# Optimization experiments

Measured on AMD Instinct MI355X. Metric: run time of the kernel, lower is better.

Reference implementation:

```python
import jax, jax.numpy as jnp
import numpy as np

FEAT, NHID, NHALF, NCLS = 256, 512, 256, 2

def _xavier(key, shape):
    fan_in, fan_out = shape[0], shape[1]
    limit = np.sqrt(6.0 / (fan_in + fan_out))
    return jax.random.uniform(key, shape, jnp.float32, -limit, limit)

def setup_inputs() -> dict:
    key = jax.random.key(0)
    ks = jax.random.split(key, 10)
    B, N = 64, 1024
    x = jax.random.normal(ks[0], (B, N, FEAT), jnp.float32)
    adj = jax.random.uniform(ks[1], (B, N, N), jnp.float32)
    adj = adj / jnp.sum(adj, axis=-1, keepdims=True)  # row-normalized (mean aggregation)
    return {
        "x": x, "adj": adj,
        "W1": _xavier(ks[2], (2 * FEAT, NHID)), "b1": jnp.zeros((NHID,), jnp.float32),
        "W2": _xavier(ks[3], (2 * NHID, NHID)), "b2": jnp.zeros((NHID,), jnp.float32),
        "W3": _xavier(ks[4], (2 * NHID, NHALF)), "b3": jnp.zeros((NHALF,), jnp.float32),
        "W4": _xavier(ks[5], (2 * NHALF, NHALF)), "b4": jnp.zeros((NHALF,), jnp.float32),
        "Wc1": _xavier(ks[6], (NHALF, NHALF)), "bc1": jnp.zeros((NHALF,), jnp.float32),
        "alpha": jnp.full((NHALF,), 0.25, jnp.float32),  # PReLU per-channel slope
        "Wc2": _xavier(ks[7], (NHALF, NCLS)), "bc2": jnp.zeros((NCLS,), jnp.float32),
    }

def _gconv(x, adj, W, b):
    # MeanAggregator: bmm(adj, x); GraphConv: relu(cat([x, agg]) @ W + b)
    agg = jnp.einsum('bnm,bmd->bnd', adj, x)
    cat = jnp.concatenate([x, agg], axis=-1)
    return jax.nn.relu(jnp.einsum('bnd,df->bnf', cat, W) + b)

def reference(x, adj, W1, b1, W2, b2, W3, b3, W4, b4, Wc1, bc1, alpha, Wc2, bc2):
    h = _gconv(x, adj, W1, b1)
    h = _gconv(h, adj, W2, b2)
    h = _gconv(h, adj, W3, b3)
    h = _gconv(h, adj, W4, b4)
    h = h.reshape(-1, h.shape[-1])  # [B*N, nhid_half]
    h = h @ Wc1 + bc1
    h = jnp.where(h > 0, h, alpha * h)  # PReLU
    logits = h @ Wc2 + bc2
    return jax.nn.log_softmax(logits, axis=-1)
```

## Files before the change

kernel.cpp:

```cpp
#include <hip/hip_runtime.h>
#include <hip/hip_bf16.h>
#include <cmath>

typedef _Float16 f16;
typedef __attribute__((ext_vector_type(4))) _Float16 f16x4;
typedef __attribute__((ext_vector_type(8))) _Float16 f16x8;
typedef __attribute__((ext_vector_type(4))) float f32x4;

__device__ inline void gload_lds16(const f16* g, f16* l) {
  __builtin_amdgcn_global_load_lds(
      (const __attribute__((address_space(1))) unsigned int*)g,
      (__attribute__((address_space(3))) unsigned int*)l, 16, 0, 0);
}

__global__ __launch_bounds__(256) void cvt_f32_f16(const float* __restrict__ in,
                                                   f16* __restrict__ out, long n) {
  long stride = (long)gridDim.x * 256 * 8;
  for (long i = ((long)blockIdx.x * 256 + threadIdx.x) * 8; i < n; i += stride) {
    float4 a = *(const float4*)(in + i);
    float4 b = *(const float4*)(in + i + 4);
    f16x8 o;
    o[0] = (f16)a.x; o[1] = (f16)a.y; o[2] = (f16)a.z; o[3] = (f16)a.w;
    o[4] = (f16)b.x; o[5] = (f16)b.y; o[6] = (f16)b.z; o[7] = (f16)b.w;
    *(f16x8*)(out + i) = o;
  }
}

__global__ __launch_bounds__(256) void transpose_cvt(const float* __restrict__ in,
                                                     f16* __restrict__ out,
                                                     int R, int C, long sIn, long sOut) {
  in  += (long)blockIdx.z * sIn;
  out += (long)blockIdx.z * sOut;
  __shared__ f16 t[32][34];
  const int tx = threadIdx.x, ty = threadIdx.y;
  const int c0 = blockIdx.x * 32, r0 = blockIdx.y * 32;
  #pragma unroll
  for (int j = 0; j < 32; j += 8)
    t[ty + j][tx] = (f16)in[(long)(r0 + ty + j) * C + (c0 + tx)];
  __syncthreads();
  #pragma unroll
  for (int j = 0; j < 32; j += 8)
    out[(long)(c0 + ty + j) * R + (r0 + tx)] = t[tx][ty + j];
}

template <int ACT, bool DUAL, bool WRITE_T>
__global__ __launch_bounds__(512, 2) void gemm256(
    const f16* __restrict__ A1, int lda1,
    const f16* __restrict__ B1, int ldb1, int k1,
    const f16* __restrict__ A2, int lda2,
    const f16* __restrict__ B2, int ldb2, int k2,
    const float* __restrict__ bias, const float* __restrict__ alpha,
    f16* __restrict__ C, int ldc, f16* __restrict__ CT,
    long sA, long sB, long sC) {
  __shared__ f16 As[2][16384];
  __shared__ f16 Bs[2][16384];
  const int tid = threadIdx.x;
  const int z = blockIdx.z;
  const f16* a1 = A1 + (long)z * sA;
  const f16* b1 = B1 + (long)z * sB;
  f16* pC = C + (long)z * sC;
  const int m0 = blockIdx.x * 256, n0 = blockIdx.y * 256;
  const int lane = tid & 63, w = tid >> 6;
  const int wr = w >> 2, wc = w & 3;
  const int lrow = lane & 15, kg = lane >> 4;
  const int NT1 = k1 >> 6;
  const int NT = NT1 + (DUAL ? (k2 >> 6) : 0);

  const int srow = tid >> 3;
  const int cg = (tid & 7) ^ (srow & 7);
  const int ldst = (tid & 448) * 8;

  const int swz = lrow & 7;
  const int ac0 = ((0 * 4 + kg) ^ swz) * 8;
  const int ac1 = ((4 + kg) ^ swz) * 8;
  const int arow = wr * 128 + lrow;
  const int brow = wc * 64 + lrow;

  f32x4 acc[8][4] = {};

  auto stage = [&](int kt) {
    const f16 *Ab, *Bb; int la, lb, kk;
    if (!DUAL || kt < NT1) { Ab = a1; Bb = b1; la = lda1; lb = ldb1; kk = kt << 6; }
    else { Ab = A2; Bb = B2; la = lda2; lb = ldb2; kk = (kt - NT1) << 6; }
    const int bs = kt & 1;
    #pragma unroll
    for (int j = 0; j < 4; ++j)
      gload_lds16(Ab + (long)(m0 + srow + j * 64) * la + kk + cg * 8,
                  &As[bs][j * 4096 + ldst]);
    #pragma unroll
    for (int j = 0; j < 4; ++j)
      gload_lds16(Bb + (long)(n0 + srow + j * 64) * lb + kk + cg * 8,
                  &Bs[bs][j * 4096 + ldst]);
  };

  stage(0);
  stage(1);
  asm volatile("s_waitcnt vmcnt(8)\n\ts_barrier" ::: "memory");

  for (int t = 0; t < NT; ++t) {
    const int bs = t & 1;
    f16x8 af[8], bf[4];
    #pragma unroll
    for (int m = 0; m < 8; ++m)
      af[m] = *(const f16x8*)&As[bs][(arow + m * 16) * 64 + ac0];
    #pragma unroll
    for (int n = 0; n < 4; ++n)
      bf[n] = *(const f16x8*)&Bs[bs][(brow + n * 16) * 64 + ac0];
    __builtin_amdgcn_s_setprio(1);
    #pragma unroll
    for (int m = 0; m < 8; ++m)
      #pragma unroll
      for (int n = 0; n < 4; ++n)
        acc[m][n] = __builtin_amdgcn_mfma_f32_16x16x32_f16(af[m], bf[n], acc[m][n], 0, 0, 0);
    __builtin_amdgcn_s_setprio(0);
    f16x8 ag[8], bg[4];
    #pragma unroll
    for (int m = 0; m < 8; ++m)
      ag[m] = *(const f16x8*)&As[bs][(arow + m * 16) * 64 + ac1];
    #pragma unroll
    for (int n = 0; n < 4; ++n)
      bg[n] = *(const f16x8*)&Bs[bs][(brow + n * 16) * 64 + ac1];
    asm volatile("s_waitcnt lgkmcnt(0)\n\ts_barrier" ::: "memory");
    if (t + 2 < NT) stage(t + 2);
    __builtin_amdgcn_s_setprio(1);
    #pragma unroll
    for (int m = 0; m < 8; ++m)
      #pragma unroll
      for (int n = 0; n < 4; ++n)
        acc[m][n] = __builtin_amdgcn_mfma_f32_16x16x32_f16(ag[m], bg[n], acc[m][n], 0, 0, 0);
    __builtin_amdgcn_s_setprio(0);
    if (t + 2 < NT)
      asm volatile("s_waitcnt vmcnt(8)\n\ts_barrier" ::: "memory");
    else if (t + 1 < NT)
      asm volatile("s_waitcnt vmcnt(0)\n\ts_barrier" ::: "memory");
  }

  #pragma unroll
  for (int n = 0; n < 4; ++n) {
    const int gn = n0 + wc * 64 + n * 16 + lrow;
    const float bv = bias ? bias[gn] : 0.0f;
    const float av = (ACT == 2) ? alpha[gn] : 0.0f;
    #pragma unroll
    for (int m = 0; m < 8; ++m) {
      const int rg0 = m0 + wr * 128 + m * 16 + kg * 4;
      f16 tv[4];
      #pragma unroll
      for (int r = 0; r < 4; ++r) {
        float v = acc[m][n][r] + bv;
        if (ACT == 1) v = fmaxf(v, 0.0f);
        if (ACT == 2) v = (v > 0.0f) ? v : av * v;
        const f16 h = (f16)v;
        tv[r] = h;
        pC[(long)(rg0 + r) * ldc + gn] = h;
      }
      if (WRITE_T) {
        const int b = rg0 >> 10, node = rg0 & 1023;
        f16x4 pk;
        pk[0] = tv[0]; pk[1] = tv[1]; pk[2] = tv[2]; pk[3] = tv[3];
        *(f16x4*)&CT[((long)b * ldc + gn) * 1024 + node] = pk;
      }
    }
  }
}

__global__ __launch_bounds__(256) void logits_lsm(const f16* __restrict__ hc,
                                                  const float* __restrict__ Wc2,
                                                  const float* __restrict__ bc2,
                                                  float* __restrict__ out) {
  __shared__ float w[512];
  __shared__ float bb[2];
  const int t = threadIdx.x;
  w[t] = Wc2[t];
  w[t + 256] = Wc2[t + 256];
  if (t < 2) bb[t] = bc2[t];
  __syncthreads();
  const long row = (long)blockIdx.x * 256 + t;
  const f16* hr = hc + row * 256;
  float l0 = 0.f, l1 = 0.f;
  #pragma unroll 4
  for (int d0 = 0; d0 < 256; d0 += 8) {
    f16x8 v = *(const f16x8*)(hr + d0);
    #pragma unroll
    for (int j = 0; j < 8; ++j) {
      const float p = (float)v[j];
      l0 += p * w[(d0 + j) * 2];
      l1 += p * w[(d0 + j) * 2 + 1];
    }
  }
  l0 += bb[0];
  l1 += bb[1];
  const float mx = fmaxf(l0, l1);
  const float lse = mx + logf(expf(l0 - mx) + expf(l1 - mx));
  out[row * 2] = l0 - lse;
  out[row * 2 + 1] = l1 - lse;
}

extern "C" void kernel_launch(void* const* d_in, const int* in_sizes, int n_in,
                              void* d_out, int out_size, void* d_ws, size_t ws_size,
                              hipStream_t stream) {
  const float* x     = (const float*)d_in[0];
  const float* adj   = (const float*)d_in[1];
  const float* W1    = (const float*)d_in[2];
  const float* b1    = (const float*)d_in[3];
  const float* W2    = (const float*)d_in[4];
  const float* b2    = (const float*)d_in[5];
  const float* W3    = (const float*)d_in[6];
  const float* b3    = (const float*)d_in[7];
  const float* W4    = (const float*)d_in[8];
  const float* b4    = (const float*)d_in[9];
  const float* Wc1   = (const float*)d_in[10];
  const float* bc1   = (const float*)d_in[11];
  const float* alpha = (const float*)d_in[12];
  const float* Wc2   = (const float*)d_in[13];
  const float* bc2   = (const float*)d_in[14];
  float* out = (float*)d_out;

  char* ws = (char*)d_ws;
  f16* adjB = (f16*)(ws + 0L);
  f16* xN   = (f16*)(ws + 134217728L);
  f16* xT   = (f16*)(ws + 167772160L);
  f16* agg  = (f16*)(ws + 201326592L);
  f16* hAN  = (f16*)(ws + 268435456L);
  f16* hAT  = (f16*)(ws + 335544320L);
  f16* hBN  = (f16*)(ws + 402653184L);
  f16* hBT  = (f16*)(ws + 469762048L);
  f16* WT1  = (f16*)(ws + 536870912L);
  f16* WT2  = (f16*)(ws + 537395200L);
  f16* WT3  = (f16*)(ws + 538443776L);
  f16* WT4  = (f16*)(ws + 538968064L);
  f16* WTc1 = (f16*)(ws + 539230208L);
  if (ws_size < (size_t)539361280L) return;

  const dim3 tb(32, 8, 1);

  cvt_f32_f16<<<2048, 256, 0, stream>>>(adj, adjB, 64L * 1024 * 1024);
  cvt_f32_f16<<<1024, 256, 0, stream>>>(x, xN, 64L * 1024 * 256);
  transpose_cvt<<<dim3(8, 32, 64), tb, 0, stream>>>(x, xT, 1024, 256, 1024L * 256, 256L * 1024);
  transpose_cvt<<<dim3(16, 16, 1), tb, 0, stream>>>(W1, WT1, 512, 512, 0, 0);
  transpose_cvt<<<dim3(16, 32, 1), tb, 0, stream>>>(W2, WT2, 1024, 512, 0, 0);
  transpose_cvt<<<dim3(8, 32, 1), tb, 0, stream>>>(W3, WT3, 1024, 256, 0, 0);
  transpose_cvt<<<dim3(8, 16, 1), tb, 0, stream>>>(W4, WT4, 512, 256, 0, 0);
  transpose_cvt<<<dim3(8, 8, 1), tb, 0, stream>>>(Wc1, WTc1, 256, 256, 0, 0);

  gemm256<0, false, false><<<dim3(4, 1, 64), 512, 0, stream>>>(
      adjB, 1024, xT, 1024, 1024,
      nullptr, 0, nullptr, 0, 0,
      nullptr, nullptr, agg, 256, nullptr,
      1024L * 1024, 256L * 1024, 1024L * 256);
  gemm256<1, true, true><<<dim3(256, 2, 1), 512, 0, stream>>>(
      xN, 256, WT1, 512, 256,
      agg, 256, WT1 + 256, 512, 256,
      b1, nullptr, hAN, 512, hAT, 0, 0, 0);

  gemm256<0, false, false><<<dim3(4, 2, 64), 512, 0, stream>>>(
      adjB, 1024, hAT, 1024, 1024,
      nullptr, 0, nullptr, 0, 0,
      nullptr, nullptr, agg, 512, nullptr,
      1024L * 1024, 512L * 1024, 1024L * 512);
  gemm256<1, true, true><<<dim3(256, 2, 1), 512, 0, stream>>>(
      hAN, 512, WT2, 1024, 512,
      agg, 512, WT2 + 512, 1024, 512,
      b2, nullptr, hBN, 512, hBT, 0, 0, 0);

  gemm256<0, false, false><<<dim3(4, 2, 64), 512, 0, stream>>>(
      adjB, 1024, hBT, 1024, 1024,
      nullptr, 0, nullptr, 0, 0,
      nullptr, nullptr, agg, 512, nullptr,
      1024L * 1024, 512L * 1024, 1024L * 512);
  gemm256<1, true, true><<<dim3(256, 1, 1), 512, 0, stream>>>(
      hBN, 512, WT3, 1024, 512,
      agg, 512, WT3 + 512, 1024, 512,
      b3, nullptr, hAN, 256, hAT, 0, 0, 0);

  gemm256<0, false, false><<<dim3(4, 1, 64), 512, 0, stream>>>(
      adjB, 1024, hAT, 1024, 1024,
      nullptr, 0, nullptr, 0, 0,
      nullptr, nullptr, agg, 256, nullptr,
      1024L * 1024, 256L * 1024, 1024L * 256);
  gemm256<1, true, false><<<dim3(256, 1, 1), 512, 0, stream>>>(
      hAN, 256, WT4, 512, 256,
      agg, 256, WT4 + 256, 512, 256,
      b4, nullptr, hBN, 256, nullptr, 0, 0, 0);

  gemm256<2, false, false><<<dim3(256, 1, 1), 512, 0, stream>>>(
      hBN, 256, WTc1, 256, 256,
      nullptr, 0, nullptr, 0, 0,
      bc1, alpha, hAN, 256, nullptr, 0, 0, 0);

  logits_lsm<<<256, 256, 0, stream>>>(hAN, Wc2, bc2, out);
}
```

Measured before the change: 1.125 ms.

## Restructure GEMM main loop into four barrier-synced phases and remap workgroups across XCDs

The GEMM main loop now runs in four smaller phases, each doing a 4x4 MFMA block with its own LDS fragment reads. A and B tile loads are issued at different points in the loop so global-to-LDS traffic overlaps with compute, and the barrier/waitcnt pattern keeps waves in lockstep. The grid is flattened to 1D and block IDs are remapped so consecutive tiles of the same batch and row land on the same XCD, which should improve L2 reuse. The cost is many more barriers per iteration and fewer fragments held in registers at once, so latency hiding may suffer.

New measurement: 1.134 ms. No clear change (+0.8%).

```diff
diff --git a/kernel.cpp b/kernel.cpp
--- a/kernel.cpp
+++ b/kernel.cpp
@@ -43,6 +43,23 @@
     out[(long)(c0 + ty + j) * R + (r0 + tx)] = t[tx][ty + j];
 }
 
+#define MM16(AF, BF, MB)                                                        \
+  do {                                                                          \
+    __builtin_amdgcn_s_setprio(1);                                              \
+    _Pragma("unroll") for (int m_ = 0; m_ < 4; ++m_)                            \
+        _Pragma("unroll") for (int n_ = 0; n_ < 4; ++n_)                        \
+            acc[(MB) + m_][n_] = __builtin_amdgcn_mfma_f32_16x16x32_f16(        \
+                (AF)[m_], (BF)[n_], acc[(MB) + m_][n_], 0, 0, 0);               \
+    __builtin_amdgcn_s_setprio(0);                                              \
+  } while (0)
+
+#define PHASE_SYNC()                                                            \
+  do {                                                                          \
+    __builtin_amdgcn_s_barrier();                                               \
+    asm volatile("s_waitcnt lgkmcnt(0)" ::: "memory");                          \
+    __builtin_amdgcn_sched_barrier(0);                                          \
+  } while (0)
+
 template <int ACT, bool DUAL, bool WRITE_T>
 __global__ __launch_bounds__(512, 2) void gemm256(
     const f16* __restrict__ A1, int lda1,
@@ -51,15 +68,20 @@
     const f16* __restrict__ B2, int ldb2, int k2,
     const float* __restrict__ bias, const float* __restrict__ alpha,
     f16* __restrict__ C, int ldc, f16* __restrict__ CT,
-    long sA, long sB, long sC) {
-  __shared__ f16 As[2][16384];
-  __shared__ f16 Bs[2][16384];
+    long sA, long sB, long sC, int gxs, int gys, int nwg) {
+  __shared__ __align__(16) f16 As[2][16384];
+  __shared__ __align__(16) f16 Bs[2][16384];
+  const int wg = blockIdx.x;
+  const int lid = (wg & 7) * (nwg >> 3) + (wg >> 3);
+  const int bx = lid & ((1 << gxs) - 1);
+  const int by = (lid >> gxs) & ((1 << gys) - 1);
+  const int z = lid >> (gxs + gys);
+
   const int tid = threadIdx.x;
-  const int z = blockIdx.z;
   const f16* a1 = A1 + (long)z * sA;
   const f16* b1 = B1 + (long)z * sB;
   f16* pC = C + (long)z * sC;
-  const int m0 = blockIdx.x * 256, n0 = blockIdx.y * 256;
+  const int m0 = bx * 256, n0 = by * 256;
   const int lane = tid & 63, w = tid >> 6;
   const int wr = w >> 2, wc = w & 3;
   const int lrow = lane & 15, kg = lane >> 4;
@@ -71,68 +93,77 @@
   const int ldst = (tid & 448) * 8;
 
   const int swz = lrow & 7;
-  const int ac0 = ((0 * 4 + kg) ^ swz) * 8;
+  const int ac0 = (kg ^ swz) * 8;
   const int ac1 = ((4 + kg) ^ swz) * 8;
   const int arow = wr * 128 + lrow;
   const int brow = wc * 64 + lrow;
 
   f32x4 acc[8][4] = {};
-
-  auto stage = [&](int kt) {
-    const f16 *Ab, *Bb; int la, lb, kk;
-    if (!DUAL || kt < NT1) { Ab = a1; Bb = b1; la = lda1; lb = ldb1; kk = kt << 6; }
-    else { Ab = A2; Bb = B2; la = lda2; lb = ldb2; kk = (kt - NT1) << 6; }
-    const int bs = kt & 1;
+  int bs = 0;
+
+  auto stageA = [&](int kt) {
+    const f16* Ab; int la, kk;
+    if (!DUAL || kt < NT1) { Ab = a1; la = lda1; kk = kt << 6; }
+    else { Ab = A2; la = lda2; kk = (kt - NT1) << 6; }
+    const int b = kt & 1;
     #pragma unroll
     for (int j = 0; j < 4; ++j)
       gload_lds16(Ab + (long)(m0 + srow + j * 64) * la + kk + cg * 8,
-                  &As[bs][j * 4096 + ldst]);
+                  &As[b][j * 4096 + ldst]);
+  };
+  auto stageB = [&](int kt) {
+    const f16* Bb; int lb, kk;
+    if (!DUAL || kt < NT1) { Bb = b1; lb = ldb1; kk = kt << 6; }
+    else { Bb = B2; lb = ldb2; kk = (kt - NT1) << 6; }
+    const int b = kt & 1;
     #pragma unroll
     for (int j = 0; j < 4; ++j)
       gload_lds16(Bb + (long)(n0 + srow + j * 64) * lb + kk + cg * 8,
-                  &Bs[bs][j * 4096 + ldst]);
+                  &Bs[b][j * 4096 + ldst]);
   };
-
-  stage(0);
-  stage(1);
-  asm volatile("s_waitcnt vmcnt(8)\n\ts_barrier" ::: "memory");
+  auto rdB = [&](f16x8* bf, int ac) {
+    #pragma unroll
+    for (int n = 0; n < 4; ++n)
+      bf[n] = *(const f16x8*)&Bs[bs][(brow + n * 16) * 64 + ac];
+  };
+  auto rdA = [&](f16x8* af, int mo, int ac) {
+    #pragma unroll
+    for (int m = 0; m < 4; ++m)
+      af[m] = *(const f16x8*)&As[bs][(arow + mo + m * 16) * 64 + ac];
+  };
+
+  stageA(0); stageB(0); stageB(1);
+  asm volatile("s_waitcnt vmcnt(4)" ::: "memory");
+  __builtin_amdgcn_s_barrier();
 
   for (int t = 0; t < NT; ++t) {
-    const int bs = t & 1;
-    f16x8 af[8], bf[4];
-    #pragma unroll
-    for (int m = 0; m < 8; ++m)
-      af[m] = *(const f16x8*)&As[bs][(arow + m * 16) * 64 + ac0];
-    #pragma unroll
-    for (int n = 0; n < 4; ++n)
-      bf[n] = *(const f16x8*)&Bs[bs][(brow + n * 16) * 64 + ac0];
-    __builtin_amdgcn_s_setprio(1);
-    #pragma unroll
-    for (int m = 0; m < 8; ++m)
-      #pragma unroll
-      for (int n = 0; n < 4; ++n)
-        acc[m][n] = __builtin_amdgcn_mfma_f32_16x16x32_f16(af[m], bf[n], acc[m][n], 0, 0, 0);
-    __builtin_amdgcn_s_setprio(0);
-    f16x8 ag[8], bg[4];
-    #pragma unroll
-    for (int m = 0; m < 8; ++m)
-      ag[m] = *(const f16x8*)&As[bs][(arow + m * 16) * 64 + ac1];
-    #pragma unroll
-    for (int n = 0; n < 4; ++n)
-      bg[n] = *(const f16x8*)&Bs[bs][(brow + n * 16) * 64 + ac1];
-    asm volatile("s_waitcnt lgkmcnt(0)\n\ts_barrier" ::: "memory");
-    if (t + 2 < NT) stage(t + 2);
-    __builtin_amdgcn_s_setprio(1);
-    #pragma unroll
-    for (int m = 0; m < 8; ++m)
-      #pragma unroll
-      for (int n = 0; n < 4; ++n)
-        acc[m][n] = __builtin_amdgcn_mfma_f32_16x16x32_f16(ag[m], bg[n], acc[m][n], 0, 0, 0);
-    __builtin_amdgcn_s_setprio(0);
-    if (t + 2 < NT)
-      asm volatile("s_waitcnt vmcnt(8)\n\ts_barrier" ::: "memory");
-    else if (t + 1 < NT)
-      asm volatile("s_waitcnt vmcnt(0)\n\ts_barrier" ::: "memory");
+    bs = t & 1;
+    f16x8 bf0[4], bf1[4], af[4];
+    if (t + 1 < NT) stageA(t + 1);
+    rdB(bf0, ac0); rdA(af, 0, ac0);
+    PHASE_SYNC();
+    MM16(af, bf0, 0);
+    __builtin_amdgcn_s_barrier();
+    rdB(bf1, ac1); rdA(af, 0, ac1);
+    PHASE_SYNC();
+    MM16(af, bf1, 0);
+    __builtin_amdgcn_s_barrier();
+    if (t + 2 < NT) stageB(t + 2);
+    rdA(af, 64, ac0);
+    PHASE_SYNC();
+    MM16(af, bf0, 4);
+    __builtin_amdgcn_s_barrier();
+    rdA(af, 64, ac1);
+    PHASE_SYNC();
+    MM16(af, bf1, 4);
+    __builtin_amdgcn_s_barrier();
+    if (t + 1 < NT) {
+      if (t + 2 < NT)
+        asm volatile("s_waitcnt vmcnt(4)" ::: "memory");
+      else
+        asm volatile("s_waitcnt vmcnt(0)" ::: "memory");
+      __builtin_amdgcn_s_barrier();
+    }
   }
 
   #pragma unroll
@@ -242,50 +273,50 @@
   transpose_cvt<<<dim3(8, 16, 1), tb, 0, stream>>>(W4, WT4, 512, 256, 0, 0);
   transpose_cvt<<<dim3(8, 8, 1), tb, 0, stream>>>(Wc1, WTc1, 256, 256, 0, 0);
 
-  gemm256<0, false, false><<<dim3(4, 1, 64), 512, 0, stream>>>(
+  gemm256<0, false, false><<<256, 512, 0, stream>>>(
       adjB, 1024, xT, 1024, 1024,
       nullptr, 0, nullptr, 0, 0,
       nullptr, nullptr, agg, 256, nullptr,
-      1024L * 1024, 256L * 1024, 1024L * 256);
-  gemm256<1, true, true><<<dim3(256, 2, 1), 512, 0, stream>>>(
+      1024L * 1024, 256L * 1024, 1024L * 256, 2, 0, 256);
+  gemm256<1, true, true><<<512, 512, 0, stream>>>(
       xN, 256, WT1, 512, 256,
       agg, 256, WT1 + 256, 512, 256,
-      b1, nullptr, hAN, 512, hAT, 0, 0, 0);
-
-  gemm256<0, false, false><<<dim3(4, 2, 64), 512, 0, stream>>>(
+      b1, nullptr, hAN, 512, hAT, 0, 0, 0, 8, 1, 512);
+
+  gemm256<0, false, false><<<512, 512, 0, stream>>>(
       adjB, 1024, hAT, 1024, 1024,
       nullptr, 0, nullptr, 0, 0,
       nullptr, nullptr, agg, 512, nullptr,
-      1024L * 1024, 512L * 1024, 1024L * 512);
-  gemm256<1, true, true><<<dim3(256, 2, 1), 512, 0, stream>>>(
+      1024L * 1024, 512L * 1024, 1024L * 512, 2, 1, 512);
+  gemm256<1, true, true><<<512, 512, 0, stream>>>(
       hAN, 512, WT2, 1024, 512,
       agg, 512, WT2 + 512, 1024, 512,
-      b2, nullptr, hBN, 512, hBT, 0, 0, 0);
-
-  gemm256<0, false, false><<<dim3(4, 2, 64), 512, 0, stream>>>(
+      b2, nullptr, hBN, 512, hBT, 0, 0, 0, 8, 1, 512);
+
+  gemm256<0, false, false><<<512, 512, 0, stream>>>(
       adjB, 1024, hBT, 1024, 1024,
       nullptr, 0, nullptr, 0, 0,
       nullptr, nullptr, agg, 512, nullptr,
-      1024L * 1024, 512L * 1024, 1024L * 512);
-  gemm256<1, true, true><<<dim3(256, 1, 1), 512, 0, stream>>>(
+      1024L * 1024, 512L * 1024, 1024L * 512, 2, 1, 512);
+  gemm256<1, true, true><<<256, 512, 0, stream>>>(
       hBN, 512, WT3, 1024, 512,
       agg, 512, WT3 + 512, 1024, 512,
-      b3, nullptr, hAN, 256, hAT, 0, 0, 0);
-
-  gemm256<0, false, false><<<dim3(4, 1, 64), 512, 0, stream>>>(
+      b3, nullptr, hAN, 256, hAT, 0, 0, 0, 8, 0, 256);
+
+  gemm256<0, false, false><<<256, 512, 0, stream>>>(
       adjB, 1024, hAT, 1024, 1024,
       nullptr, 0, nullptr, 0, 0,
       nullptr, nullptr, agg, 256, nullptr,
-      1024L * 1024, 256L * 1024, 1024L * 256);
-  gemm256<1, true, false><<<dim3(256, 1, 1), 512, 0, stream>>>(
+      1024L * 1024, 256L * 1024, 1024L * 256, 2, 0, 256);
+  gemm256<1, true, false><<<256, 512, 0, stream>>>(
       hAN, 256, WT4, 512, 256,
       agg, 256, WT4 + 256, 512, 256,
-      b4, nullptr, hBN, 256, nullptr, 0, 0, 0);
-
-  gemm256<2, false, false><<<dim3(256, 1, 1), 512, 0, stream>>>(
+      b4, nullptr, hBN, 256, nullptr, 0, 0, 0, 8, 0, 256);
+
+  gemm256<2, false, false><<<256, 512, 0, stream>>>(
       hBN, 256, WTc1, 256, 256,
       nullptr, 0, nullptr, 0, 0,
-      bc1, alpha, hAN, 256, nullptr, 0, 0, 0);
+      bc1, alpha, hAN, 256, nullptr, 0, 0, 0, 8, 0, 256);
 
   logits_lsm<<<256, 256, 0, stream>>>(hAN, Wc2, bc2, out);
 }
```
